# Kernel tuning notes

Measured on AMD Instinct MI355X. Metric: run time of the kernel, lower is better.

## Reference

```python
import jax, jax.numpy as jnp
import numpy as np

START_IDX = 1
PAD_IDX = 0
VOCAB, EMB, HID, FEAT = 32000, 256, 512, 1024
B, T = 32, 100


def setup_inputs() -> dict:
    key = jax.random.key(0)
    ks = jax.random.split(key, 12)
    features = jax.random.normal(ks[0], (B, FEAT, 7, 7), dtype=jnp.float32)
    reports = jax.random.randint(ks[1], (B, T), 0, VOCAB)
    emb_table = jax.random.normal(ks[2], (VOCAB, EMB), dtype=jnp.float32) * 0.02
    emb_table = emb_table.at[PAD_IDX].set(0.0)  # padding_idx row is zero
    fc_w = jax.random.normal(ks[3], (HID, FEAT), dtype=jnp.float32) * 0.02
    fc_b = jnp.zeros((HID,), dtype=jnp.float32)
    W_ih = jax.random.normal(ks[4], (4 * HID, EMB), dtype=jnp.float32) * 0.02
    b_ih = jnp.zeros((4 * HID,), dtype=jnp.float32)
    W_hh = jax.random.normal(ks[5], (4 * HID, HID), dtype=jnp.float32) * 0.02
    b_hh = jnp.zeros((4 * HID,), dtype=jnp.float32)
    Wv = jax.random.normal(ks[6], (VOCAB, HID), dtype=jnp.float32) * 0.02
    bv = jnp.zeros((VOCAB,), dtype=jnp.float32)
    return {"features": features, "reports": reports, "emb_table": emb_table,
            "fc_w": fc_w, "fc_b": fc_b, "W_ih": W_ih, "b_ih": b_ih,
            "W_hh": W_hh, "b_hh": b_hh, "Wv": Wv, "bv": bv}


def reference(features, reports, emb_table, fc_w, fc_b, W_ih, b_ih, W_hh, b_hh, Wv, bv):
    bsz = features.shape[0]
    # features_fc: AdaptiveAvgPool2d((1,1)) + Flatten + Linear
    pooled = features.mean(axis=(2, 3))                       # (B, FEAT)
    h0 = pooled @ fc_w.T + fc_b                               # (B, HID)
    c0 = jnp.zeros_like(h0)
    # teacher forcing: inputs are [START, reports[:, :-1]]
    tok = jnp.concatenate(
        [jnp.full((bsz, 1), START_IDX, dtype=reports.dtype), reports[:, :-1]], axis=1)
    xs = emb_table[tok].transpose(1, 0, 2)                    # (T, B, EMB)

    def step(carry, x_t):
        h, c = carry
        gates = x_t @ W_ih.T + b_ih + h @ W_hh.T + b_hh       # (B, 4*HID)
        i, f, g, o = jnp.split(gates, 4, axis=-1)             # torch gate order i,f,g,o
        i = jax.nn.sigmoid(i)
        f = jax.nn.sigmoid(f)
        g = jnp.tanh(g)
        o = jax.nn.sigmoid(o)
        c = f * c + i * g
        h = o * jnp.tanh(c)
        logits = h @ Wv.T + bv                                # (B, VOCAB)
        return (h, c), logits

    _, logits = jax.lax.scan(step, (h0, c0), xs)              # (T, B, VOCAB)
    return (logits.transpose(1, 0, 2),)                       # (B, T, VOCAB)
```

## Files before the change

### kernel.cpp

```cpp
#include <hip/hip_runtime.h>
#include <math.h>

#define T_STEPS 100
#define BATCH   32
#define EMB     256
#define HID     512
#define FEATC   1024
#define VOCAB   32000
#define GATES   2048
#define M_ROWS  (T_STEPS * BATCH)

typedef __attribute__((ext_vector_type(8))) short bf16x8;
typedef __attribute__((ext_vector_type(4))) float f32x4;
typedef unsigned short ushort_t;

__device__ __forceinline__ unsigned short f2bf(float x) {
  union { float f; unsigned u; } v; v.f = x;
  unsigned r = v.u + 0x7fff + ((v.u >> 16) & 1);
  return (unsigned short)(r >> 16);
}
__device__ __forceinline__ float bf2f(unsigned short h) {
  union { float f; unsigned u; } v; v.u = ((unsigned)h) << 16;
  return v.f;
}

__global__ __launch_bounds__(512) void pool_fc_kernel(
    const float* __restrict__ features, const float* __restrict__ fc_w,
    const float* __restrict__ fc_b, float* __restrict__ h0) {
  __shared__ float pooled_s[FEATC];
  const int b = blockIdx.x;
  const int tid = threadIdx.x;
  const float* fb = features + (size_t)b * FEATC * 49;
  for (int f = tid; f < FEATC; f += 512) {
    const float* p = fb + f * 49;
    float s = 0.f;
#pragma unroll
    for (int i = 0; i < 49; ++i) s += p[i];
    pooled_s[f] = s / 49.0f;
  }
  __syncthreads();
  const float4* w4 = (const float4*)(fc_w + (size_t)tid * FEATC);
  const float4* p4 = (const float4*)pooled_s;
  float acc = fc_b[tid];
#pragma unroll 8
  for (int k = 0; k < FEATC / 4; ++k) {
    float4 w = w4[k], p = p4[k];
    acc += w.x * p.x + w.y * p.y + w.z * p.z + w.w * p.w;
  }
  h0[b * HID + tid] = acc;
}

#define BM 128
#define BN 128
#define BK 16
#define LDP (BM + 4)

__global__ __launch_bounds__(256) void xg_gemm_kernel(
    const int* __restrict__ reports, const float* __restrict__ emb,
    const float* __restrict__ W_ih, const float* __restrict__ b_ih,
    const float* __restrict__ b_hh, float* __restrict__ xg) {
  __shared__ float As[BK][LDP];
  __shared__ float Bs[BK][LDP];
  __shared__ int rowbase_s[BM];
  const int tid = threadIdx.x;
  const int n0 = blockIdx.x * BN;
  const int m0 = blockIdx.y * BM;
  if (tid < BM) {
    int m = m0 + tid;
    int t = m >> 5, b = m & 31;
    int tok = (t == 0) ? 1 : reports[b * T_STEPS + (t - 1)];
    rowbase_s[tid] = tok * EMB;
  }
  __syncthreads();

  float acc[8][8];
#pragma unroll
  for (int i = 0; i < 8; ++i)
#pragma unroll
    for (int j = 0; j < 8; ++j) acc[i][j] = 0.f;

  const int tx = tid & 15, ty = tid >> 4;

  for (int kt = 0; kt < EMB / BK; ++kt) {
    const int k0 = kt * BK;
#pragma unroll
    for (int l = 0; l < 2; ++l) {
      int idx = l * 256 + tid;
      int rm = idx >> 2;
      int kk = (idx & 3) * 4;
      float4 av = *(const float4*)(emb + rowbase_s[rm] + k0 + kk);
      As[kk + 0][rm] = av.x; As[kk + 1][rm] = av.y;
      As[kk + 2][rm] = av.z; As[kk + 3][rm] = av.w;
      float4 bvv = *(const float4*)(W_ih + (size_t)(n0 + rm) * EMB + k0 + kk);
      Bs[kk + 0][rm] = bvv.x; Bs[kk + 1][rm] = bvv.y;
      Bs[kk + 2][rm] = bvv.z; Bs[kk + 3][rm] = bvv.w;
    }
    __syncthreads();
#pragma unroll
    for (int kk = 0; kk < BK; ++kk) {
      float a[8], bf[8];
      *(float4*)(a)     = *(const float4*)&As[kk][ty * 4];
      *(float4*)(a + 4) = *(const float4*)&As[kk][64 + ty * 4];
      *(float4*)(bf)     = *(const float4*)&Bs[kk][tx * 4];
      *(float4*)(bf + 4) = *(const float4*)&Bs[kk][64 + tx * 4];
#pragma unroll
      for (int i = 0; i < 8; ++i)
#pragma unroll
        for (int j = 0; j < 8; ++j) acc[i][j] += a[i] * bf[j];
    }
    __syncthreads();
  }

#pragma unroll
  for (int i = 0; i < 8; ++i) {
    int m = m0 + ((i < 4) ? (ty * 4 + i) : (64 + ty * 4 + i - 4));
    float* orow = xg + (size_t)m * GATES;
    int c0 = n0 + tx * 4;
    int c1 = n0 + 64 + tx * 4;
    float4 r0, r1;
    r0.x = acc[i][0] + b_ih[c0 + 0] + b_hh[c0 + 0];
    r0.y = acc[i][1] + b_ih[c0 + 1] + b_hh[c0 + 1];
    r0.z = acc[i][2] + b_ih[c0 + 2] + b_hh[c0 + 2];
    r0.w = acc[i][3] + b_ih[c0 + 3] + b_hh[c0 + 3];
    r1.x = acc[i][4] + b_ih[c1 + 0] + b_hh[c1 + 0];
    r1.y = acc[i][5] + b_ih[c1 + 1] + b_hh[c1 + 1];
    r1.z = acc[i][6] + b_ih[c1 + 2] + b_hh[c1 + 2];
    r1.w = acc[i][7] + b_ih[c1 + 3] + b_hh[c1 + 3];
    *(float4*)(orow + c0) = r0;
    *(float4*)(orow + c1) = r1;
  }
}

__global__ __launch_bounds__(256) void split_kernel(
    const float* __restrict__ x, unsigned short* __restrict__ hi,
    unsigned short* __restrict__ lo, int n4) {
  int i = blockIdx.x * 256 + threadIdx.x;
  if (i >= n4) return;
  float4 v = ((const float4*)x)[i];
  ushort4 h, l;
  h.x = f2bf(v.x); l.x = f2bf(v.x - bf2f(h.x));
  h.y = f2bf(v.y); l.y = f2bf(v.y - bf2f(h.y));
  h.z = f2bf(v.z); l.z = f2bf(v.z - bf2f(h.z));
  h.w = f2bf(v.w); l.w = f2bf(v.w - bf2f(h.w));
  ((ushort4*)hi)[i] = h;
  ((ushort4*)lo)[i] = l;
}

__global__ __launch_bounds__(1024) void lstm_step_kernel(
    const float* __restrict__ W_hh, const float* __restrict__ xg,
    float* __restrict__ hbuf, float* __restrict__ c_ws,
    unsigned short* __restrict__ Hall_hi, unsigned short* __restrict__ Hall_lo,
    int t) {
  __shared__ float hsm[4][HID];
  __shared__ float psum[1024];
  __shared__ float gsm[4][4][16];
  const int tid = threadIdx.x;
  const int j = blockIdx.x & 31;
  const int bg = blockIdx.x >> 5;

  const float* hsrc = hbuf + (t & 1) * (BATCH * HID);
  if (tid < 512) {
    int b = tid >> 7, k4 = (tid & 127) * 4;
    *(float4*)&hsm[b][k4] = *(const float4*)&hsrc[(bg * 4 + b) * HID + k4];
  }
  __syncthreads();

  const int kq = tid & 3, u = (tid >> 2) & 15, g = (tid >> 6) & 3, b = tid >> 8;
  const int row = g * HID + j * 16 + u;
  const float* wrow = W_hh + (size_t)row * HID;
  float acc = 0.f;
#pragma unroll
  for (int it = 0; it < 32; ++it) {
    int k = it * 16 + kq * 4;
    float4 wv = *(const float4*)&wrow[k];
    float4 hv = *(const float4*)&hsm[b][k];
    acc += wv.x * hv.x + wv.y * hv.y + wv.z * hv.z + wv.w * hv.w;
  }
  psum[tid] = acc;
  __syncthreads();

  if (tid < 256) {
    int u2 = tid & 15, g2 = (tid >> 4) & 3, b2 = tid >> 6;
    int base = (b2 << 8) + (g2 << 6) + (u2 << 2);
    float s = psum[base] + psum[base + 1] + psum[base + 2] + psum[base + 3];
    int row2 = g2 * HID + j * 16 + u2;
    s += xg[((size_t)t * BATCH + bg * 4 + b2) * GATES + row2];
    gsm[b2][g2][u2] = s;
  }
  __syncthreads();

  if (tid < 64) {
    int u3 = tid & 15, b3 = tid >> 4;
    float iv = gsm[b3][0][u3];
    float fv = gsm[b3][1][u3];
    float gv = gsm[b3][2][u3];
    float ov = gsm[b3][3][u3];
    float si = 1.f / (1.f + expf(-iv));
    float sf = 1.f / (1.f + expf(-fv));
    float sg = tanhf(gv);
    float so = 1.f / (1.f + expf(-ov));
    int bb = bg * 4 + b3, uu = j * 16 + u3;
    int cidx = bb * HID + uu;
    float cp = (t == 0) ? 0.f : c_ws[cidx];
    float cn = sf * cp + si * sg;
    float hn = so * tanhf(cn);
    c_ws[cidx] = cn;
    hbuf[((t + 1) & 1) * (BATCH * HID) + cidx] = hn;
    unsigned short hhi = f2bf(hn);
    unsigned short hlo = f2bf(hn - bf2f(hhi));
    size_t hidx = ((size_t)t * BATCH + bb) * HID + uu;
    Hall_hi[hidx] = hhi;
    Hall_lo[hidx] = hlo;
  }
}

__global__ __launch_bounds__(256, 2) void out_mfma_kernel(
    const unsigned short* __restrict__ Ahi, const unsigned short* __restrict__ Alo,
    const unsigned short* __restrict__ Bhi, const unsigned short* __restrict__ Blo,
    const float* __restrict__ bv, float* __restrict__ out) {
  __shared__ unsigned short Ah[128 * 32], Al[128 * 32], Bh[128 * 32], Bl[128 * 32];
  const int tid = threadIdx.x;
  const int lane = tid & 63;
  const int w = tid >> 6;
  const int wm = w & 1, wn = w >> 1;
  const int m0 = blockIdx.x * 128;
  const int n0 = blockIdx.y * 128;

  f32x4 acc[4][4] = {};

  const int srow4 = lane >> 2;
  const int skoff = ((lane & 3) ^ ((lane >> 3) & 3)) * 8;

  for (int kt = 0; kt < 16; ++kt) {
    const int k0 = kt * 32;
#pragma unroll
    for (int issue = 0; issue < 2; ++issue) {
      const int r = w * 32 + issue * 16 + srow4;
      const size_t gA = (size_t)(m0 + r) * 512 + k0 + skoff;
      const size_t gB = (size_t)(n0 + r) * 512 + k0 + skoff;
      const int loff = (w * 32 + issue * 16) * 32;
      __builtin_amdgcn_global_load_lds(
          (const __attribute__((address_space(1))) void*)(Ahi + gA),
          (__attribute__((address_space(3))) void*)(Ah + loff), 16, 0, 0);
      __builtin_amdgcn_global_load_lds(
          (const __attribute__((address_space(1))) void*)(Alo + gA),
          (__attribute__((address_space(3))) void*)(Al + loff), 16, 0, 0);
      __builtin_amdgcn_global_load_lds(
          (const __attribute__((address_space(1))) void*)(Bhi + gB),
          (__attribute__((address_space(3))) void*)(Bh + loff), 16, 0, 0);
      __builtin_amdgcn_global_load_lds(
          (const __attribute__((address_space(1))) void*)(Blo + gB),
          (__attribute__((address_space(3))) void*)(Bl + loff), 16, 0, 0);
    }
    __syncthreads();

    bf16x8 ah[4], al[4], bh[4], bl[4];
    const int q = lane >> 4;
    const int rl = lane & 15;
    const int slot = (q ^ ((rl >> 1) & 3)) * 8;
#pragma unroll
    for (int i = 0; i < 4; ++i) {
      int arow = wm * 64 + i * 16 + rl;
      ah[i] = *(const bf16x8*)&Ah[arow * 32 + slot];
      al[i] = *(const bf16x8*)&Al[arow * 32 + slot];
      int brow = wn * 64 + i * 16 + rl;
      bh[i] = *(const bf16x8*)&Bh[brow * 32 + slot];
      bl[i] = *(const bf16x8*)&Bl[brow * 32 + slot];
    }
#pragma unroll
    for (int i = 0; i < 4; ++i)
#pragma unroll
      for (int jj = 0; jj < 4; ++jj) {
        acc[i][jj] = __builtin_amdgcn_mfma_f32_16x16x32_bf16(ah[i], bh[jj], acc[i][jj], 0, 0, 0);
        acc[i][jj] = __builtin_amdgcn_mfma_f32_16x16x32_bf16(al[i], bh[jj], acc[i][jj], 0, 0, 0);
        acc[i][jj] = __builtin_amdgcn_mfma_f32_16x16x32_bf16(ah[i], bl[jj], acc[i][jj], 0, 0, 0);
      }
    __syncthreads();
  }

#pragma unroll
  for (int jj = 0; jj < 4; ++jj) {
    const int ncol = n0 + wn * 64 + jj * 16 + (lane & 15);
    const float bvn = bv[ncol];
#pragma unroll
    for (int i = 0; i < 4; ++i) {
      const int mbase = m0 + wm * 64 + i * 16 + (lane >> 4) * 4;
#pragma unroll
      for (int r = 0; r < 4; ++r) {
        const int m = mbase + r;
        const int t = m >> 5, b = m & 31;
        out[((size_t)(b * T_STEPS + t)) * VOCAB + ncol] = acc[i][jj][r] + bvn;
      }
    }
  }
}

extern "C" void kernel_launch(void* const* d_in, const int* in_sizes, int n_in,
                              void* d_out, int out_size, void* d_ws, size_t ws_size,
                              hipStream_t stream) {
  const float* features = (const float*)d_in[0];
  const int*   reports  = (const int*)d_in[1];
  const float* emb      = (const float*)d_in[2];
  const float* fc_w     = (const float*)d_in[3];
  const float* fc_b     = (const float*)d_in[4];
  const float* W_ih     = (const float*)d_in[5];
  const float* b_ih     = (const float*)d_in[6];
  const float* W_hh     = (const float*)d_in[7];
  const float* b_hh     = (const float*)d_in[8];
  const float* Wv       = (const float*)d_in[9];
  const float* bv       = (const float*)d_in[10];
  float* out = (float*)d_out;

  float* ws = (float*)d_ws;
  float* xg   = ws;
  float* hbuf = xg + (size_t)M_ROWS * GATES;
  float* c_ws = hbuf + 2 * BATCH * HID;
  unsigned short* Hall_hi = (unsigned short*)(c_ws + BATCH * HID);
  unsigned short* Hall_lo = Hall_hi + (size_t)M_ROWS * HID;
  unsigned short* Wv_hi   = Hall_lo + (size_t)M_ROWS * HID;
  unsigned short* Wv_lo   = Wv_hi + (size_t)VOCAB * HID;

  pool_fc_kernel<<<BATCH, 512, 0, stream>>>(features, fc_w, fc_b, hbuf);
  xg_gemm_kernel<<<dim3(GATES / BN, M_ROWS / BM), 256, 0, stream>>>(
      reports, emb, W_ih, b_ih, b_hh, xg);
  {
    int n4 = VOCAB * HID / 4;
    split_kernel<<<(n4 + 255) / 256, 256, 0, stream>>>(Wv, Wv_hi, Wv_lo, n4);
  }
  for (int t = 0; t < T_STEPS; ++t)
    lstm_step_kernel<<<256, 1024, 0, stream>>>(W_hh, xg, hbuf, c_ws,
                                               Hall_hi, Hall_lo, t);
  out_mfma_kernel<<<dim3(M_ROWS / 128, VOCAB / 128), 256, 0, stream>>>(
      Hall_hi, Hall_lo, Wv_hi, Wv_lo, bv, out);
}
```

Baseline: 1.752 ms.

## Replace per-step LSTM launches with persistent cooperative kernel using flag barriers

Replaces 100 separate lstm_step kernel launches with one cooperative persistent kernel of 64 workgroups. Each workgroup keeps its W_hh slice in registers as split bf16 hi/lo, computes the recurrent gates with MFMA, and syncs across workgroups through per-workgroup global flags. h is exchanged through the Hall buffers, which now hold T+1 steps, and c stays in registers. This is meant to remove launch overhead and repeated W_hh reloads, at the cost of a spin-wait barrier and a bf16x3 precision scheme for the recurrent matmul.

```diff
diff --git a/kernel.cpp b/kernel.cpp
--- a/kernel.cpp
+++ b/kernel.cpp
@@ -9,10 +9,10 @@
 #define VOCAB   32000
 #define GATES   2048
 #define M_ROWS  (T_STEPS * BATCH)
+#define NWG     64
 
 typedef __attribute__((ext_vector_type(8))) short bf16x8;
 typedef __attribute__((ext_vector_type(4))) float f32x4;
-typedef unsigned short ushort_t;
 
 __device__ __forceinline__ unsigned short f2bf(float x) {
   union { float f; unsigned u; } v; v.f = x;
@@ -26,7 +26,8 @@
 
 __global__ __launch_bounds__(512) void pool_fc_kernel(
     const float* __restrict__ features, const float* __restrict__ fc_w,
-    const float* __restrict__ fc_b, float* __restrict__ h0) {
+    const float* __restrict__ fc_b, unsigned short* __restrict__ h0_hi,
+    unsigned short* __restrict__ h0_lo) {
   __shared__ float pooled_s[FEATC];
   const int b = blockIdx.x;
   const int tid = threadIdx.x;
@@ -47,7 +48,10 @@
     float4 w = w4[k], p = p4[k];
     acc += w.x * p.x + w.y * p.y + w.z * p.z + w.w * p.w;
   }
-  h0[b * HID + tid] = acc;
+  unsigned short hh = f2bf(acc);
+  unsigned short hl = f2bf(acc - bf2f(hh));
+  h0_hi[b * HID + tid] = hh;
+  h0_lo[b * HID + tid] = hl;
 }
 
 #define BM 128
@@ -146,71 +150,132 @@
   ((ushort4*)lo)[i] = l;
 }
 
-__global__ __launch_bounds__(1024) void lstm_step_kernel(
+__global__ __launch_bounds__(256) void lstm_persist_kernel(
     const float* __restrict__ W_hh, const float* __restrict__ xg,
-    float* __restrict__ hbuf, float* __restrict__ c_ws,
     unsigned short* __restrict__ Hall_hi, unsigned short* __restrict__ Hall_lo,
-    int t) {
-  __shared__ float hsm[4][HID];
-  __shared__ float psum[1024];
-  __shared__ float gsm[4][4][16];
+    unsigned* __restrict__ flags) {
+  __shared__ float part[4][32][32];
+  __shared__ float gsm[32][32];
   const int tid = threadIdx.x;
-  const int j = blockIdx.x & 31;
-  const int bg = blockIdx.x >> 5;
-
-  const float* hsrc = hbuf + (t & 1) * (BATCH * HID);
-  if (tid < 512) {
-    int b = tid >> 7, k4 = (tid & 127) * 4;
-    *(float4*)&hsm[b][k4] = *(const float4*)&hsrc[(bg * 4 + b) * HID + k4];
-  }
-  __syncthreads();
-
-  const int kq = tid & 3, u = (tid >> 2) & 15, g = (tid >> 6) & 3, b = tid >> 8;
-  const int row = g * HID + j * 16 + u;
-  const float* wrow = W_hh + (size_t)row * HID;
-  float acc = 0.f;
-#pragma unroll
-  for (int it = 0; it < 32; ++it) {
-    int k = it * 16 + kq * 4;
-    float4 wv = *(const float4*)&wrow[k];
-    float4 hv = *(const float4*)&hsm[b][k];
-    acc += wv.x * hv.x + wv.y * hv.y + wv.z * hv.z + wv.w * hv.w;
-  }
-  psum[tid] = acc;
-  __syncthreads();
-
-  if (tid < 256) {
-    int u2 = tid & 15, g2 = (tid >> 4) & 3, b2 = tid >> 6;
-    int base = (b2 << 8) + (g2 << 6) + (u2 << 2);
-    float s = psum[base] + psum[base + 1] + psum[base + 2] + psum[base + 3];
-    int row2 = g2 * HID + j * 16 + u2;
-    s += xg[((size_t)t * BATCH + bg * 4 + b2) * GATES + row2];
-    gsm[b2][g2][u2] = s;
-  }
-  __syncthreads();
-
-  if (tid < 64) {
-    int u3 = tid & 15, b3 = tid >> 4;
-    float iv = gsm[b3][0][u3];
-    float fv = gsm[b3][1][u3];
-    float gv = gsm[b3][2][u3];
-    float ov = gsm[b3][3][u3];
-    float si = 1.f / (1.f + expf(-iv));
-    float sf = 1.f / (1.f + expf(-fv));
-    float sg = tanhf(gv);
-    float so = 1.f / (1.f + expf(-ov));
-    int bb = bg * 4 + b3, uu = j * 16 + u3;
-    int cidx = bb * HID + uu;
-    float cp = (t == 0) ? 0.f : c_ws[cidx];
-    float cn = sf * cp + si * sg;
-    float hn = so * tanhf(cn);
-    c_ws[cidx] = cn;
-    hbuf[((t + 1) & 1) * (BATCH * HID) + cidx] = hn;
-    unsigned short hhi = f2bf(hn);
-    unsigned short hlo = f2bf(hn - bf2f(hhi));
-    size_t hidx = ((size_t)t * BATCH + bb) * HID + uu;
-    Hall_hi[hidx] = hhi;
-    Hall_lo[hidx] = hlo;
+  const int wg = blockIdx.x;
+  const int w = tid >> 6;
+  const int lane = tid & 63;
+  const int rl = lane & 15;
+  const int q = lane >> 4;
+
+  bf16x8 wbh[4][2], wbl[4][2];
+#pragma unroll
+  for (int kt = 0; kt < 4; ++kt) {
+#pragma unroll
+    for (int ni = 0; ni < 2; ++ni) {
+      const int n = ni * 16 + rl;
+      const int grow = (n >> 3) * HID + wg * 8 + (n & 7);
+      const float* src = W_hh + (size_t)grow * HID + w * 128 + kt * 32 + q * 8;
+      float4 v0 = *(const float4*)(src);
+      float4 v1 = *(const float4*)(src + 4);
+      float vv[8] = {v0.x, v0.y, v0.z, v0.w, v1.x, v1.y, v1.z, v1.w};
+      bf16x8 hb, lb;
+#pragma unroll
+      for (int j = 0; j < 8; ++j) {
+        unsigned short h = f2bf(vv[j]);
+        hb[j] = (short)h;
+        lb[j] = (short)f2bf(vv[j] - bf2f(h));
+      }
+      wbh[kt][ni] = hb;
+      wbl[kt][ni] = lb;
+    }
+  }
+
+  const int ab = tid >> 3;
+  const int au = tid & 7;
+  float c_reg = 0.f;
+
+  for (int t = 0; t < T_STEPS; ++t) {
+    if (t > 0) {
+      if (tid < NWG) {
+        while (__hip_atomic_load(&flags[tid], __ATOMIC_RELAXED,
+                                 __HIP_MEMORY_SCOPE_AGENT) < (unsigned)t) {
+          __builtin_amdgcn_s_sleep(1);
+        }
+      }
+      __syncthreads();
+      __threadfence();
+    }
+
+    const unsigned short* Ah = Hall_hi + (size_t)t * (BATCH * HID);
+    const unsigned short* Al = Hall_lo + (size_t)t * (BATCH * HID);
+    f32x4 acc[2][2] = {};
+#pragma unroll
+    for (int kt = 0; kt < 4; ++kt) {
+      const int k0 = w * 128 + kt * 32 + q * 8;
+      bf16x8 ah[2], al[2];
+#pragma unroll
+      for (int mi = 0; mi < 2; ++mi) {
+        const size_t off = (size_t)(mi * 16 + rl) * HID + k0;
+        ah[mi] = *(const bf16x8*)(Ah + off);
+        al[mi] = *(const bf16x8*)(Al + off);
+      }
+#pragma unroll
+      for (int mi = 0; mi < 2; ++mi)
+#pragma unroll
+        for (int ni = 0; ni < 2; ++ni) {
+          acc[mi][ni] = __builtin_amdgcn_mfma_f32_16x16x32_bf16(ah[mi], wbh[kt][ni], acc[mi][ni], 0, 0, 0);
+          acc[mi][ni] = __builtin_amdgcn_mfma_f32_16x16x32_bf16(al[mi], wbh[kt][ni], acc[mi][ni], 0, 0, 0);
+          acc[mi][ni] = __builtin_amdgcn_mfma_f32_16x16x32_bf16(ah[mi], wbl[kt][ni], acc[mi][ni], 0, 0, 0);
+        }
+    }
+
+#pragma unroll
+    for (int mi = 0; mi < 2; ++mi)
+#pragma unroll
+      for (int ni = 0; ni < 2; ++ni)
+#pragma unroll
+        for (int r = 0; r < 4; ++r)
+          part[w][mi * 16 + q * 4 + r][ni * 16 + rl] = acc[mi][ni][r];
+    __syncthreads();
+
+    {
+      const int m = tid >> 3;
+      const int n4 = (tid & 7) * 4;
+      float4 s0 = *(float4*)&part[0][m][n4];
+      float4 s1 = *(float4*)&part[1][m][n4];
+      float4 s2 = *(float4*)&part[2][m][n4];
+      float4 s3 = *(float4*)&part[3][m][n4];
+      const float4 xv = *(const float4*)(
+          xg + ((size_t)t * BATCH + m) * GATES + (n4 >> 3) * HID + wg * 8 + (n4 & 7));
+      float4 g;
+      g.x = s0.x + s1.x + s2.x + s3.x + xv.x;
+      g.y = s0.y + s1.y + s2.y + s3.y + xv.y;
+      g.z = s0.z + s1.z + s2.z + s3.z + xv.z;
+      g.w = s0.w + s1.w + s2.w + s3.w + xv.w;
+      *(float4*)&gsm[m][n4] = g;
+    }
+    __syncthreads();
+
+    {
+      float iv = gsm[ab][au];
+      float fv = gsm[ab][8 + au];
+      float gv = gsm[ab][16 + au];
+      float ov = gsm[ab][24 + au];
+      float si = 1.f / (1.f + expf(-iv));
+      float sf = 1.f / (1.f + expf(-fv));
+      float sg = tanhf(gv);
+      float so = 1.f / (1.f + expf(-ov));
+      c_reg = sf * c_reg + si * sg;
+      float hn = so * tanhf(c_reg);
+      unsigned short hh = f2bf(hn);
+      unsigned short hl = f2bf(hn - bf2f(hh));
+      const size_t hidx = (size_t)(t + 1) * (BATCH * HID) + (size_t)ab * HID + wg * 8 + au;
+      Hall_hi[hidx] = hh;
+      Hall_lo[hidx] = hl;
+    }
+    __syncthreads();
+
+    if (tid == 0) {
+      __threadfence();
+      __hip_atomic_store(&flags[wg], (unsigned)(t + 1), __ATOMIC_RELEASE,
+                         __HIP_MEMORY_SCOPE_AGENT);
+    }
   }
 }
 
@@ -312,24 +377,29 @@
   float* out = (float*)d_out;
 
   float* ws = (float*)d_ws;
-  float* xg   = ws;
-  float* hbuf = xg + (size_t)M_ROWS * GATES;
-  float* c_ws = hbuf + 2 * BATCH * HID;
-  unsigned short* Hall_hi = (unsigned short*)(c_ws + BATCH * HID);
-  unsigned short* Hall_lo = Hall_hi + (size_t)M_ROWS * HID;
-  unsigned short* Wv_hi   = Hall_lo + (size_t)M_ROWS * HID;
+  float* xg = ws;
+  unsigned short* Hall_hi = (unsigned short*)(xg + (size_t)M_ROWS * GATES);
+  unsigned short* Hall_lo = Hall_hi + (size_t)(T_STEPS + 1) * BATCH * HID;
+  unsigned short* Wv_hi   = Hall_lo + (size_t)(T_STEPS + 1) * BATCH * HID;
   unsigned short* Wv_lo   = Wv_hi + (size_t)VOCAB * HID;
-
-  pool_fc_kernel<<<BATCH, 512, 0, stream>>>(features, fc_w, fc_b, hbuf);
+  unsigned*       flags   = (unsigned*)(Wv_lo + (size_t)VOCAB * HID);
+
+  hipMemsetAsync(flags, 0, NWG * sizeof(unsigned), stream);
+
+  pool_fc_kernel<<<BATCH, 512, 0, stream>>>(features, fc_w, fc_b, Hall_hi, Hall_lo);
   xg_gemm_kernel<<<dim3(GATES / BN, M_ROWS / BM), 256, 0, stream>>>(
       reports, emb, W_ih, b_ih, b_hh, xg);
   {
     int n4 = VOCAB * HID / 4;
     split_kernel<<<(n4 + 255) / 256, 256, 0, stream>>>(Wv, Wv_hi, Wv_lo, n4);
   }
-  for (int t = 0; t < T_STEPS; ++t)
-    lstm_step_kernel<<<256, 1024, 0, stream>>>(W_hh, xg, hbuf, c_ws,
-                                               Hall_hi, Hall_lo, t);
+  {
+    void* kargs[] = {(void*)&W_hh, (void*)&xg, (void*)&Hall_hi, (void*)&Hall_lo,
+                     (void*)&flags};
+    hipLaunchCooperativeKernel((const void*)lstm_persist_kernel, dim3(NWG),
+                               dim3(256), kargs, 0, stream);
+  }
   out_mfma_kernel<<<dim3(M_ROWS / 128, VOCAB / 128), 256, 0, stream>>>(
-      Hall_hi, Hall_lo, Wv_hi, Wv_lo, bv, out);
-}
+      Hall_hi + (size_t)BATCH * HID, Hall_lo + (size_t)BATCH * HID,
+      Wv_hi, Wv_lo, bv, out);
+}
```

New measurement: 2.160 ms. +23.3%, slower.
